# Performance work log

Measured on AMD Instinct MI355X. Metric: run time of the kernel, lower is better.

Reference implementation:

```python
import jax, jax.numpy as jnp
import numpy as np

MAX_LEN = 1024

def _make_pe():
    # matches TemporalPositionalEncoding buffer construction
    pe = np.zeros(MAX_LEN, np.float32)
    pos = np.arange(MAX_LEN, dtype=np.float64)
    d = MAX_LEN + 1e-9
    pe[0::2] = np.sin(pos[0::2] / 10000.0 ** (pos[0::2] / d))
    pe[1::2] = np.cos(pos[1::2] / 10000.0 ** (pos[1::2] / d))
    return jnp.asarray(pe, jnp.float32)


def setup_inputs() -> dict:
    key = jax.random.key(0)
    k1, k2, k3, k4, k5 = jax.random.split(key, 5)
    B, H, W, C = 16, 56, 56, 768
    sw = 4
    x = jax.random.normal(k1, (B, H, W, C), dtype=jnp.float32)
    # source inits these to zero; use small random weights so the op is non-trivial
    qkv_w = jax.random.normal(k2, (3 * sw, sw), dtype=jnp.float32) * 0.1
    qkv_b = jax.random.normal(k3, (3 * sw,), dtype=jnp.float32) * 0.1
    proj_w = jax.random.normal(k4, (C, C), dtype=jnp.float32) * 0.02
    proj_b = jax.random.normal(k5, (C,), dtype=jnp.float32) * 0.02
    pe = _make_pe()
    return {"x": x, "qkv_w": qkv_w, "qkv_b": qkv_b,
            "proj_w": proj_w, "proj_b": proj_b, "pe": pe}


def reference(x, qkv_w, qkv_b, proj_w, proj_b, pe):
    B, H, W, C = x.shape
    sw = qkv_w.shape[0] // 3  # group_size
    # temporal positional encoding along channel dim
    x = x + pe[:C].astype(x.dtype).reshape(1, 1, 1, -1)
    pad = (-C) % sw  # static Python int
    if pad:
        x = jnp.pad(x, ((0, 0), (0, 0), (0, 0), (0, pad)))
    Cp = x.shape[-1]
    N = Cp // sw
    xg = x.reshape(B * H * W, N, sw)  # [G, N, sw]
    qkv = xg @ qkv_w.T + qkv_b        # [G, N, 3*sw]
    q, k, v = jnp.split(qkv, 3, axis=-1)
    # SDPA with q,k,v of shape [G, N, 1, sw]: seq length (L=S=1) attention.
    # softmax over the single key is identically 1, so out == v; we keep the
    # explicit score/softmax for structural fidelity (it's scalar-per-group).
    scale = 1.0 / jnp.sqrt(jnp.asarray(sw, x.dtype))
    scores = jnp.einsum('gnd,gnd->gn', q, k) * scale          # [G, N]
    attn = jax.nn.softmax(scores[..., None, None], axis=-1)   # [G, N, 1, 1] == 1
    out = attn[..., 0] * v                                    # [G, N, sw]
    out = out.reshape(B, H, W, Cp)[..., :C]
    return out @ proj_w.T + proj_b
```

## Files before the change

### kernel.cpp

```cpp
#include <hip/hip_runtime.h>
#include <hip/hip_bf16.h>

typedef __attribute__((ext_vector_type(8))) short bf16x8;
typedef __attribute__((ext_vector_type(4))) float f32x4;
typedef __attribute__((ext_vector_type(4))) unsigned short u16x4;
typedef unsigned short u16;

#define M_DIM 50176
#define N_DIM 768
#define K_DIM 768
#define XB_ELEMS ((size_t)M_DIM * K_DIM)

__device__ __forceinline__ u16 f2bf(float f) {
    __hip_bfloat16 h = __float2bfloat16(f);
    return *reinterpret_cast<u16*>(&h);
}

__device__ __forceinline__ void gld_lds16(const void* g, void* l) {
    __builtin_amdgcn_global_load_lds(
        (const __attribute__((address_space(1))) unsigned int*)g,
        (__attribute__((address_space(3))) unsigned int*)l, 16, 0, 0);
}

__global__ __launch_bounds__(256)
void cvt_x(const float* __restrict__ X, u16* __restrict__ Xb) {
    const size_t n8 = XB_ELEMS / 8;
    for (size_t i = (size_t)blockIdx.x * blockDim.x + threadIdx.x; i < n8;
         i += (size_t)gridDim.x * blockDim.x) {
        const float4* src = (const float4*)(X + i * 8);
        float4 a = src[0], b = src[1];
        u16x4 lo, hi;
        lo.x = f2bf(a.x); lo.y = f2bf(a.y); lo.z = f2bf(a.z); lo.w = f2bf(a.w);
        hi.x = f2bf(b.x); hi.y = f2bf(b.y); hi.z = f2bf(b.z); hi.w = f2bf(b.w);
        u16x4* dst = (u16x4*)(Xb + i * 8);
        dst[0] = lo;
        dst[1] = hi;
    }
}

__global__ void fold_weights(const float* __restrict__ qkv_w,
                             const float* __restrict__ qkv_b,
                             const float* __restrict__ proj_w,
                             const float* __restrict__ proj_b,
                             const float* __restrict__ pe,
                             u16* __restrict__ Bw, float* __restrict__ bias) {
    const int o = blockIdx.x;
    const int t = threadIdx.x;
    __shared__ float wv[16];
    __shared__ float bv4[4];
    __shared__ float red[4];
    if (t < 16) wv[t] = qkv_w[32 + t];
    if (t < 4)  bv4[t] = qkv_b[8 + t];
    __syncthreads();
    const float* Prow = proj_w + o * 768;
    float s = 0.f;
    for (int c = t; c < 768; c += 256) {
        int g4 = c & ~3, j = c & 3;
        float af = Prow[g4 + 0] * wv[0 * 4 + j] + Prow[g4 + 1] * wv[1 * 4 + j] +
                   Prow[g4 + 2] * wv[2 * 4 + j] + Prow[g4 + 3] * wv[3 * 4 + j];
        Bw[o * 768 + c] = f2bf(af);
        s += af * pe[c];
        s += Prow[c] * bv4[j];
    }
    #pragma unroll
    for (int off = 32; off; off >>= 1) s += __shfl_down(s, off, 64);
    if ((t & 63) == 0) red[t >> 6] = s;
    __syncthreads();
    if (t == 0) bias[o] = red[0] + red[1] + red[2] + red[3] + proj_b[o];
}

__global__ __launch_bounds__(256, 4)
void gemm_bf16(const u16* __restrict__ Xb, const u16* __restrict__ Bw,
               const float* __restrict__ bias, float* __restrict__ Y) {
    const int b = blockIdx.x;
    const int bid = (b & 7) * 294 + (b >> 3);
    const int mt = bid / 6, nt = bid - mt * 6;
    const int m0 = mt * 128, n0 = nt * 128;

    const int tid = threadIdx.x;
    const int lane = tid & 63;
    const int w = tid >> 6;
    const int wm = w >> 1, wn = w & 1;

    __shared__ u16 As[128 * 64];
    __shared__ u16 Bs[128 * 64];

    f32x4 acc[4][4];
    #pragma unroll
    for (int i = 0; i < 4; ++i)
        #pragma unroll
        for (int j = 0; j < 4; ++j)
            acc[i][j] = (f32x4){0.f, 0.f, 0.f, 0.f};

    const int bg = lane & 7;

    auto stage = [&](const u16* srcbase, u16* lds, int k0) {
        #pragma unroll
        for (int j = 0; j < 4; ++j) {
            int rowbase = j * 32 + w * 8;
            int row = rowbase + (lane >> 3);
            const char* src = (const char*)srcbase + ((long)row * K_DIM + k0) * 2 +
                              ((bg * 16) ^ ((row & 7) << 4));
            gld_lds16(src, (void*)&lds[rowbase * 64]);
        }
    };

    auto compute = [&]() {
        #pragma unroll
        for (int h = 0; h < 2; ++h) {
            bf16x8 av[4], bv_[4];
            #pragma unroll
            for (int mf = 0; mf < 4; ++mf) {
                int r = wm * 64 + mf * 16 + (lane & 15);
                int pb = (h * 64 + ((lane >> 4) << 4)) ^ ((r & 7) << 4);
                av[mf] = *(const bf16x8*)&As[r * 64 + (pb >> 1)];
            }
            #pragma unroll
            for (int nf = 0; nf < 4; ++nf) {
                int r = wn * 64 + nf * 16 + (lane & 15);
                int pb = (h * 64 + ((lane >> 4) << 4)) ^ ((r & 7) << 4);
                bv_[nf] = *(const bf16x8*)&Bs[r * 64 + (pb >> 1)];
            }
            __builtin_amdgcn_s_setprio(1);
            #pragma unroll
            for (int mf = 0; mf < 4; ++mf)
                #pragma unroll
                for (int nf = 0; nf < 4; ++nf)
                    acc[mf][nf] = __builtin_amdgcn_mfma_f32_16x16x32_bf16(
                        av[mf], bv_[nf], acc[mf][nf], 0, 0, 0);
            __builtin_amdgcn_s_setprio(0);
        }
    };

    const u16* Abase = Xb + (long)m0 * K_DIM;
    const u16* Bbase = Bw + (long)n0 * K_DIM;

    stage(Abase, As, 0);
    stage(Bbase, Bs, 0);
    __syncthreads();

    const int NT = K_DIM / 64;
    #pragma unroll 1
    for (int t = 0; t < NT - 1; ++t) {
        compute();
        __syncthreads();
        stage(Abase, As, (t + 1) * 64);
        stage(Bbase, Bs, (t + 1) * 64);
        __syncthreads();
    }
    compute();

    const int colq = lane & 15;
    const int rowq = (lane >> 4) * 4;
    #pragma unroll
    for (int nf = 0; nf < 4; ++nf) {
        int col = n0 + wn * 64 + nf * 16 + colq;
        float bi = bias[col];
        #pragma unroll
        for (int mf = 0; mf < 4; ++mf) {
            long rbase = m0 + wm * 64 + mf * 16 + rowq;
            #pragma unroll
            for (int r = 0; r < 4; ++r) {
                __builtin_nontemporal_store(acc[mf][nf][r] + bi,
                                            &Y[(rbase + r) * N_DIM + col]);
            }
        }
    }
}

__global__ __launch_bounds__(256, 2)
void gemm_fused(const float* __restrict__ X, const u16* __restrict__ Bw,
                const float* __restrict__ bias, float* __restrict__ Y) {
    const int b = blockIdx.x;
    const int bid = (b & 7) * 294 + (b >> 3);
    const int mt = bid / 6, nt = bid - mt * 6;
    const int m0 = mt * 128, n0 = nt * 128;

    const int tid = threadIdx.x;
    const int lane = tid & 63;
    const int w = tid >> 6;
    const int wm = w >> 1, wn = w & 1;

    __shared__ u16 As[2][128 * 64];
    __shared__ u16 Bs[2][128 * 64];

    f32x4 acc[4][4];
    #pragma unroll
    for (int i = 0; i < 4; ++i)
        #pragma unroll
        for (int j = 0; j < 4; ++j)
            acc[i][j] = (f32x4){0.f, 0.f, 0.f, 0.f};

    const int arow = tid >> 4;
    const int agg  = tid & 15;
    const int bg = lane & 7;

    float4 preA[8], preB[8];

    auto load_a = [&](float4 (&p)[8], int k0) {
        const float4* src = (const float4*)(X + (long)m0 * K_DIM + k0);
        #pragma unroll
        for (int i = 0; i < 8; ++i) {
            int r = arow + 16 * i;
            p[i] = src[(long)r * (K_DIM / 4) + agg];
        }
    };

    auto write_a = [&](int buf, const float4 (&p)[8]) {
        #pragma unroll
        for (int i = 0; i < 8; ++i) {
            int r = arow + 16 * i;
            int pb = (agg * 8) ^ ((r & 7) << 4);
            u16x4 hv;
            hv.x = f2bf(p[i].x);
            hv.y = f2bf(p[i].y);
            hv.z = f2bf(p[i].z);
            hv.w = f2bf(p[i].w);
            *(u16x4*)&As[buf][r * 64 + (pb >> 1)] = hv;
        }
    };

    auto stage_b = [&](int buf, int k0) {
        #pragma unroll
        for (int j = 0; j < 4; ++j) {
            int rowbase = j * 32 + w * 8;
            int row = rowbase + (lane >> 3);
            const char* src = (const char*)Bw + ((long)(n0 + row) * K_DIM + k0) * 2 +
                              ((bg * 16) ^ ((row & 7) << 4));
            gld_lds16(src, (void*)&Bs[buf][rowbase * 64]);
        }
    };

    auto compute = [&](int buf) {
        #pragma unroll
        for (int h = 0; h < 2; ++h) {
            bf16x8 av[4], bv_[4];
            #pragma unroll
            for (int mf = 0; mf < 4; ++mf) {
                int r = wm * 64 + mf * 16 + (lane & 15);
                int pb = (h * 64 + ((lane >> 4) << 4)) ^ ((r & 7) << 4);
                av[mf] = *(const bf16x8*)&As[buf][r * 64 + (pb >> 1)];
            }
            #pragma unroll
            for (int nf = 0; nf < 4; ++nf) {
                int r = wn * 64 + nf * 16 + (lane & 15);
                int pb = (h * 64 + ((lane >> 4) << 4)) ^ ((r & 7) << 4);
                bv_[nf] = *(const bf16x8*)&Bs[buf][r * 64 + (pb >> 1)];
            }
            __builtin_amdgcn_s_setprio(1);
            #pragma unroll
            for (int mf = 0; mf < 4; ++mf)
                #pragma unroll
                for (int nf = 0; nf < 4; ++nf)
                    acc[mf][nf] = __builtin_amdgcn_mfma_f32_16x16x32_bf16(
                        av[mf], bv_[nf], acc[mf][nf], 0, 0, 0);
            __builtin_amdgcn_s_setprio(0);
        }
    };

    load_a(preA, 0);
    stage_b(0, 0);
    load_a(preB, 64);
    write_a(0, preA);
    __syncthreads();

    const int NT = K_DIM / 64;
    #pragma unroll 1
    for (int t2 = 0; t2 < NT; t2 += 2) {
        if (t2 + 1 < NT) {
            write_a(1, preB);
            stage_b(1, (t2 + 1) * 64);
        }
        if (t2 + 2 < NT) load_a(preA, (t2 + 2) * 64);
        compute(0);
        __syncthreads();

        if (t2 + 2 < NT) {
            write_a(0, preA);
            stage_b(0, (t2 + 2) * 64);
        }
        if (t2 + 3 < NT) load_a(preB, (t2 + 3) * 64);
        compute(1);
        __syncthreads();
    }

    const int colq = lane & 15;
    const int rowq = (lane >> 4) * 4;
    #pragma unroll
    for (int nf = 0; nf < 4; ++nf) {
        int col = n0 + wn * 64 + nf * 16 + colq;
        float bi = bias[col];
        #pragma unroll
        for (int mf = 0; mf < 4; ++mf) {
            long rbase = m0 + wm * 64 + mf * 16 + rowq;
            #pragma unroll
            for (int r = 0; r < 4; ++r) {
                __builtin_nontemporal_store(acc[mf][nf][r] + bi,
                                            &Y[(rbase + r) * N_DIM + col]);
            }
        }
    }
}

extern "C" void kernel_launch(void* const* d_in, const int* in_sizes, int n_in,
                              void* d_out, int out_size, void* d_ws, size_t ws_size,
                              hipStream_t stream) {
    const float* x      = (const float*)d_in[0];
    const float* qkv_w  = (const float*)d_in[1];
    const float* qkv_b  = (const float*)d_in[2];
    const float* proj_w = (const float*)d_in[3];
    const float* proj_b = (const float*)d_in[4];
    const float* pe     = (const float*)d_in[5];
    float* y = (float*)d_out;

    const size_t xb_bytes   = XB_ELEMS * 2;
    const size_t bw_bytes   = (size_t)N_DIM * K_DIM * 2;
    const size_t bias_bytes = N_DIM * sizeof(float);

    if (ws_size >= xb_bytes + bw_bytes + bias_bytes) {
        u16*   Xb   = (u16*)d_ws;
        u16*   Bw   = (u16*)((char*)d_ws + xb_bytes);
        float* bias = (float*)((char*)d_ws + xb_bytes + bw_bytes);
        fold_weights<<<768, 256, 0, stream>>>(qkv_w, qkv_b, proj_w, proj_b, pe, Bw, bias);
        cvt_x<<<2048, 256, 0, stream>>>(x, Xb);
        gemm_bf16<<<(M_DIM / 128) * (N_DIM / 128), 256, 0, stream>>>(Xb, Bw, bias, y);
    } else {
        u16*   Bw   = (u16*)d_ws;
        float* bias = (float*)((char*)d_ws + bw_bytes);
        fold_weights<<<768, 256, 0, stream>>>(qkv_w, qkv_b, proj_w, proj_b, pe, Bw, bias);
        gemm_fused<<<(M_DIM / 128) * (N_DIM / 128), 256, 0, stream>>>(x, Bw, bias, y);
    }
}
```

Measured before the change: 117.6 us.

## Stage GEMM epilogue through LDS for coalesced 16-byte output stores

Both GEMM kernels now reuse shared memory as an fp32 staging pool in the epilogue. Accumulators plus bias are written with an XOR swizzle, then read back and stored to global memory as contiguous 16-byte vectors. This replaces the scattered scalar stores with row-contiguous writes. The bf16 kernel has only 32KB of LDS, so it writes the tile in two halves, adding extra barriers. The launch code also reorders cvt_x ahead of fold_weights and doubles its grid size.

```diff
diff --git a/kernel.cpp b/kernel.cpp
--- a/kernel.cpp
+++ b/kernel.cpp
@@ -82,8 +82,10 @@
     const int w = tid >> 6;
     const int wm = w >> 1, wn = w & 1;
 
-    __shared__ u16 As[128 * 64];
-    __shared__ u16 Bs[128 * 64];
+    __shared__ __align__(16) char smem[32768];
+    u16*   As   = (u16*)smem;
+    u16*   Bs   = (u16*)(smem + 16384);
+    float* pool = (float*)smem;
 
     f32x4 acc[4][4];
     #pragma unroll
@@ -149,22 +151,40 @@
         __syncthreads();
     }
     compute();
+    __syncthreads();
 
     const int colq = lane & 15;
     const int rowq = (lane >> 4) * 4;
     #pragma unroll
-    for (int nf = 0; nf < 4; ++nf) {
-        int col = n0 + wn * 64 + nf * 16 + colq;
-        float bi = bias[col];
-        #pragma unroll
-        for (int mf = 0; mf < 4; ++mf) {
-            long rbase = m0 + wm * 64 + mf * 16 + rowq;
-            #pragma unroll
-            for (int r = 0; r < 4; ++r) {
-                __builtin_nontemporal_store(acc[mf][nf][r] + bi,
-                                            &Y[(rbase + r) * N_DIM + col]);
-            }
-        }
+    for (int h = 0; h < 2; ++h) {
+        if (wm == h) {
+            #pragma unroll
+            for (int nf = 0; nf < 4; ++nf) {
+                int col = wn * 64 + nf * 16 + colq;
+                float bi = bias[n0 + col];
+                #pragma unroll
+                for (int mf = 0; mf < 4; ++mf) {
+                    #pragma unroll
+                    for (int r = 0; r < 4; ++r) {
+                        int rl = mf * 16 + rowq + r;
+                        int colS = col ^ (((rl >> 2) & 1) << 4);
+                        pool[rl * 128 + colS] = acc[mf][nf][r] + bi;
+                    }
+                }
+            }
+        }
+        __syncthreads();
+        #pragma unroll
+        for (int i = 0; i < 8; ++i) {
+            int chunk = i * 256 + tid;
+            int rl = chunk >> 5;
+            int g = chunk & 31;
+            int gs = g ^ (((rl >> 2) & 1) << 2);
+            f32x4 v = *(const f32x4*)&pool[rl * 128 + gs * 4];
+            __builtin_nontemporal_store(v,
+                (f32x4*)&Y[(long)(m0 + h * 64 + rl) * N_DIM + n0 + g * 4]);
+        }
+        if (h == 0) __syncthreads();
     }
 }
 
@@ -181,8 +201,9 @@
     const int w = tid >> 6;
     const int wm = w >> 1, wn = w & 1;
 
-    __shared__ u16 As[2][128 * 64];
-    __shared__ u16 Bs[2][128 * 64];
+    __shared__ __align__(16) float pool[16384];
+    u16 (*As)[128 * 64] = (u16(*)[128 * 64])pool;
+    u16 (*Bs)[128 * 64] = (u16(*)[128 * 64])((char*)pool + 32768);
 
     f32x4 acc[4][4];
     #pragma unroll
@@ -288,17 +309,30 @@
     const int rowq = (lane >> 4) * 4;
     #pragma unroll
     for (int nf = 0; nf < 4; ++nf) {
-        int col = n0 + wn * 64 + nf * 16 + colq;
-        float bi = bias[col];
+        int col = wn * 64 + nf * 16 + colq;
+        float bi = bias[n0 + col];
         #pragma unroll
         for (int mf = 0; mf < 4; ++mf) {
-            long rbase = m0 + wm * 64 + mf * 16 + rowq;
+            int rbase = wm * 64 + mf * 16 + rowq;
             #pragma unroll
             for (int r = 0; r < 4; ++r) {
-                __builtin_nontemporal_store(acc[mf][nf][r] + bi,
-                                            &Y[(rbase + r) * N_DIM + col]);
-            }
-        }
+                int row = rbase + r;
+                int colS = col ^ (((row >> 2) & 1) << 4);
+                pool[row * 128 + colS] = acc[mf][nf][r] + bi;
+            }
+        }
+    }
+    __syncthreads();
+
+    #pragma unroll
+    for (int i = 0; i < 16; ++i) {
+        int chunk = i * 256 + tid;
+        int row = chunk >> 5;
+        int g = chunk & 31;
+        int gs = g ^ (((row >> 2) & 1) << 2);
+        f32x4 v = *(const f32x4*)&pool[row * 128 + gs * 4];
+        __builtin_nontemporal_store(v,
+            (f32x4*)&Y[(long)(m0 + row) * N_DIM + n0 + g * 4]);
     }
 }
 
@@ -321,8 +355,8 @@
         u16*   Xb   = (u16*)d_ws;
         u16*   Bw   = (u16*)((char*)d_ws + xb_bytes);
         float* bias = (float*)((char*)d_ws + xb_bytes + bw_bytes);
+        cvt_x<<<4096, 256, 0, stream>>>(x, Xb);
         fold_weights<<<768, 256, 0, stream>>>(qkv_w, qkv_b, proj_w, proj_b, pe, Bw, bias);
-        cvt_x<<<2048, 256, 0, stream>>>(x, Xb);
         gemm_bf16<<<(M_DIM / 128) * (N_DIM / 128), 256, 0, stream>>>(Xb, Bw, bias, y);
     } else {
         u16*   Bw   = (u16*)d_ws;
```

After: 110.4 us. -6.1%, faster.
